# Optimization experiments

Measured on AMD Instinct MI355X. Metric: run time of the kernel, lower is better.

## Reference

```python
import jax, jax.numpy as jnp
import numpy as np

T, F, H = 2048, 256, 384  # seq_len, input_size, hidden_size


def setup_inputs() -> dict:
    key = jax.random.key(0)
    ks = jax.random.split(key, 16)
    s = 1.0 / np.sqrt(F)
    d = {"x": jax.random.normal(ks[0], (T, F), jnp.float32)}
    names = ["q", "k", "v", "i", "f", "o"]
    for j, n in enumerate(names):
        d[f"W{n}"] = jax.random.uniform(ks[1 + j], (H, F), jnp.float32, -s, s)
        d[f"b{n}"] = jax.random.uniform(ks[7 + j], (H,), jnp.float32, -s, s)
    d["conv_w"] = jax.random.uniform(ks[13], (1, 1, 4), jnp.float32, -0.5, 0.5)
    d["conv_b"] = jax.random.uniform(ks[14], (1,), jnp.float32, -0.5, 0.5)
    return d


def _forward(x, Wq, bq, Wk, bk, Wv, bv, Wi, bi, Wf, bf, Wo, bo, conv_w, conv_b):
    # Conv1d(1->1, kernel=4, padding=(3,3)) along time, per input feature.
    xt = x.T[:, None, :]  # (F, 1, T)  feature axis acts as batch
    y = jax.lax.conv_general_dilated(xt, conv_w, (1,), [(3, 3)])  # (F, 1, T+3)
    xp = (y[:, 0, :] + conv_b[0]).T  # (T+3, F)

    inv_sqrt_h = 1.0 / jnp.sqrt(jnp.asarray(H, xp.dtype))
    # Precompute all per-step projections with dense GEMMs (time-parallel part).
    q = xp @ Wq.T + bq                      # (T+3, H)
    k = (xp @ Wk.T + bk) * inv_sqrt_h       # (T+3, H); extra bias_k is zero-init
    v = xp @ Wv.T + bv
    i = jnp.exp(xp @ Wi.T + bi)
    f = jax.nn.sigmoid(xp @ Wf.T + bf)
    o = jax.nn.sigmoid(xp @ Wo.T + bo)

    def step(carry, inp):
        C, n = carry                         # C: (H,H), n: (H,)
        qt, kt, vt, it, ft, ot = inp
        C = ft * C + it * jnp.outer(vt, kt)  # broadcast over last axis, as original
        n = ft * n + it * kt
        den = jnp.maximum(jnp.abs(jnp.dot(n, qt)), 1.0)
        h = ot * (C @ qt) / den
        return (C, n), h

    init = (jnp.zeros((H, H), xp.dtype), jnp.zeros((H,), xp.dtype))
    _, hs = jax.lax.scan(step, init, (q, k, v, i, f, o))
    return hs[-1]  # return_all=False -> last hidden state, shape (H,)


def reference(x, Wq, bq, Wk, bk, Wv, bv, Wi, bi, Wf, bf, Wo, bo, conv_w, conv_b):
    return _forward(x, Wq, bq, Wk, bk, Wv, bv, Wi, bi, Wf, bf, Wo, bo, conv_w, conv_b)
```

## Files before the change

kernel.cpp:

```cpp
#include <hip/hip_runtime.h>
#include <math.h>

#define T_IN 2048
#define TP   2051
#define F    256
#define H    384
#define BK   16
#define NT2  129
#define NCS  258
#define NC3  257

__device__ __forceinline__ float logsig(float z) {
    return (z >= 0.0f) ? -log1pf(__expf(-z)) : z - log1pf(__expf(z));
}

__global__ __launch_bounds__(256) void k1_conv(const float* __restrict__ x,
                        const float* __restrict__ cw,
                        const float* __restrict__ cb, float* __restrict__ xp) {
    int t = blockIdx.x * 4 + (threadIdx.x >> 6);
    int f4 = threadIdx.x & 63;
    if (t >= TP) return;
    float w[4] = {cw[0], cw[1], cw[2], cw[3]};
    float b = cb[0];
    float4 acc = {b, b, b, b};
    int i0 = t - 3;
    const float4* x4 = (const float4*)x;
    #pragma unroll
    for (int j = 0; j < 4; ++j) {
        int tt = i0 + j;
        if (tt >= 0 && tt < T_IN) {
            float4 xv = x4[tt * 64 + f4];
            acc.x = fmaf(w[j], xv.x, acc.x);
            acc.y = fmaf(w[j], xv.y, acc.y);
            acc.z = fmaf(w[j], xv.z, acc.z);
            acc.w = fmaf(w[j], xv.w, acc.w);
        }
    }
    ((float4*)xp)[t * 64 + f4] = acc;
}

__global__ __launch_bounds__(64) void k2_proj(
    const float* __restrict__ xp,
    const float* __restrict__ Wk, const float* __restrict__ bk,
    const float* __restrict__ Wi, const float* __restrict__ bi,
    const float* __restrict__ Wf, const float* __restrict__ bf,
    float* __restrict__ zk, float* __restrict__ ai, float* __restrict__ lf,
    float* __restrict__ cs) {
    __shared__ float alds[BK][20];
    __shared__ float wlds[3][BK][68];
    __shared__ float csred[4][68];
    int tid = threadIdx.x;
    int t0 = blockIdx.x * 16, b0 = blockIdx.y * 64;
    int tx = tid & 15, ty = tid >> 4;
    const float* Wg[3] = {Wk, Wi, Wf};
    float acc[3][16];
    #pragma unroll
    for (int j = 0; j < 3; ++j)
        #pragma unroll
        for (int u = 0; u < 16; ++u) acc[j][u] = 0.0f;

    int at = tid >> 2;
    int ak = (tid & 3) * 4;

    for (int k0 = 0; k0 < 256; k0 += BK) {
        __syncthreads();
        float4 xv = {0.f, 0.f, 0.f, 0.f};
        if (t0 + at < TP) xv = *(const float4*)&xp[(t0 + at) * 256 + k0 + ak];
        alds[ak + 0][at] = xv.x; alds[ak + 1][at] = xv.y;
        alds[ak + 2][at] = xv.z; alds[ak + 3][at] = xv.w;
        #pragma unroll
        for (int j = 0; j < 3; ++j) {
            #pragma unroll
            for (int h = 0; h < 4; ++h) {
                int row = h * 16 + at;
                float4 wv = *(const float4*)&Wg[j][(b0 + row) * 256 + k0 + ak];
                wlds[j][ak + 0][row] = wv.x; wlds[j][ak + 1][row] = wv.y;
                wlds[j][ak + 2][row] = wv.z; wlds[j][ak + 3][row] = wv.w;
            }
        }
        __syncthreads();
        #pragma unroll
        for (int kk = 0; kk < BK; ++kk) {
            float4 a4 = *(const float4*)&alds[kk][ty * 4];
            #pragma unroll
            for (int j = 0; j < 3; ++j) {
                float4 b4 = *(const float4*)&wlds[j][kk][tx * 4];
                acc[j][0]  = fmaf(a4.x, b4.x, acc[j][0]);
                acc[j][1]  = fmaf(a4.x, b4.y, acc[j][1]);
                acc[j][2]  = fmaf(a4.x, b4.z, acc[j][2]);
                acc[j][3]  = fmaf(a4.x, b4.w, acc[j][3]);
                acc[j][4]  = fmaf(a4.y, b4.x, acc[j][4]);
                acc[j][5]  = fmaf(a4.y, b4.y, acc[j][5]);
                acc[j][6]  = fmaf(a4.y, b4.z, acc[j][6]);
                acc[j][7]  = fmaf(a4.y, b4.w, acc[j][7]);
                acc[j][8]  = fmaf(a4.z, b4.x, acc[j][8]);
                acc[j][9]  = fmaf(a4.z, b4.y, acc[j][9]);
                acc[j][10] = fmaf(a4.z, b4.z, acc[j][10]);
                acc[j][11] = fmaf(a4.z, b4.w, acc[j][11]);
                acc[j][12] = fmaf(a4.w, b4.x, acc[j][12]);
                acc[j][13] = fmaf(a4.w, b4.y, acc[j][13]);
                acc[j][14] = fmaf(a4.w, b4.z, acc[j][14]);
                acc[j][15] = fmaf(a4.w, b4.w, acc[j][15]);
            }
        }
    }
    int bA = b0 + tx * 4;
    float4 bk4 = *(const float4*)&bk[bA];
    float4 bi4 = *(const float4*)&bi[bA];
    float4 bf4 = *(const float4*)&bf[bA];
    const float sc = 0.05103103630798287f;
    float4 lfs = {0.f, 0.f, 0.f, 0.f};
    #pragma unroll
    for (int tt = 0; tt < 4; ++tt) {
        int t = t0 + ty * 4 + tt;
        if (t < TP) {
            int row = t * H + bA;
            int o = tt * 4;
            float4 v;
            v.x = (acc[0][o+0] + bk4.x) * sc; v.y = (acc[0][o+1] + bk4.y) * sc;
            v.z = (acc[0][o+2] + bk4.z) * sc; v.w = (acc[0][o+3] + bk4.w) * sc;
            *(float4*)&zk[row] = v;
            v.x = acc[1][o+0] + bi4.x; v.y = acc[1][o+1] + bi4.y;
            v.z = acc[1][o+2] + bi4.z; v.w = acc[1][o+3] + bi4.w;
            *(float4*)&ai[row] = v;
            float4 l;
            l.x = logsig(acc[2][o+0] + bf4.x); l.y = logsig(acc[2][o+1] + bf4.y);
            l.z = logsig(acc[2][o+2] + bf4.z); l.w = logsig(acc[2][o+3] + bf4.w);
            *(float4*)&lf[row] = l;
            lfs.x += l.x; lfs.y += l.y; lfs.z += l.z; lfs.w += l.w;
        }
    }
    *(float4*)&csred[ty][tx * 4] = lfs;
    __syncthreads();
    {
        float s0 = csred[0][tid] + csred[1][tid];
        float s1 = csred[2][tid] + csred[3][tid];
        cs[(2 * blockIdx.x + 0) * H + b0 + tid] = s0;
        cs[(2 * blockIdx.x + 1) * H + b0 + tid] = s1;
    }
}

__global__ __launch_bounds__(256) void k2b_qo(const float* __restrict__ xp,
        const float* __restrict__ Wq, const float* __restrict__ bq,
        const float* __restrict__ Wo, const float* __restrict__ bo,
        float* __restrict__ q, float* __restrict__ o) {
    int tid = threadIdx.x;
    int lane = tid & 63;
    int row = blockIdx.x * 4 + (tid >> 6);
    float4 xv = *(const float4*)&xp[(TP - 1) * 256 + lane * 4];
    float4 q4 = *(const float4*)&Wq[row * 256 + lane * 4];
    float4 o4 = *(const float4*)&Wo[row * 256 + lane * 4];
    float aq = fmaf(xv.x, q4.x, fmaf(xv.y, q4.y, fmaf(xv.z, q4.z, xv.w * q4.w)));
    float ao = fmaf(xv.x, o4.x, fmaf(xv.y, o4.y, fmaf(xv.z, o4.z, xv.w * o4.w)));
    #pragma unroll
    for (int off = 32; off; off >>= 1) {
        aq += __shfl_down(aq, off, 64);
        ao += __shfl_down(ao, off, 64);
    }
    if (lane == 0) {
        q[row] = aq + bq[row];
        o[row] = 1.0f / (1.0f + __expf(-(ao + bo[row])));
    }
}

__global__ __launch_bounds__(64) void k3b_scan(const float* __restrict__ cs,
                                               float* __restrict__ co) {
    int b = blockIdx.x * 64 + threadIdx.x;
    float L = 0.0f;
    #pragma unroll 16
    for (int c = NCS - 1; c >= 0; --c) {
        co[c * H + b] = L;
        L += cs[c * H + b];
    }
}

__global__ __launch_bounds__(384) void k3_fused(
    const float* __restrict__ ai, const float* __restrict__ lf,
    const float* __restrict__ zk, const float* __restrict__ co,
    const float* __restrict__ q, const float* __restrict__ xp,
    float* __restrict__ zf, float* __restrict__ Gf) {
    __shared__ float zred[6][256];
    __shared__ float gred[6];
    int tid = threadIdx.x;
    int w = tid >> 6, lane = tid & 63;
    int c = blockIdx.x, ts = c * 8;
    float co0 = co[c * H + tid];
    float qb = q[tid];
    float aiv[8], lfv[8], zkv[8];
    float4 xv[8];
    if (ts + 8 <= TP) {
        #pragma unroll
        for (int u = 0; u < 8; ++u) {
            int idx = (ts + u) * H + tid;
            aiv[u] = ai[idx]; lfv[u] = lf[idx]; zkv[u] = zk[idx];
            xv[u] = *(const float4*)&xp[(ts + u) * 256 + lane * 4];
        }
    } else {
        #pragma unroll
        for (int u = 0; u < 8; ++u) {
            if (ts + u < TP) {
                int idx = (ts + u) * H + tid;
                aiv[u] = ai[idx]; lfv[u] = lf[idx]; zkv[u] = zk[idx];
                xv[u] = *(const float4*)&xp[(ts + u) * 256 + lane * 4];
            } else {
                aiv[u] = -1e30f; lfv[u] = 0.f; zkv[u] = 0.f;
                xv[u].x = xv[u].y = xv[u].z = xv[u].w = 0.f;
            }
        }
    }
    float S = 0.f, gsum = 0.f;
    float z0 = 0.f, z1 = 0.f, z2 = 0.f, z3 = 0.f;
    #pragma unroll
    for (int u = 7; u >= 0; --u) {
        float wv = __expf(aiv[u] + co0 + S) * zkv[u] * qb;
        S += lfv[u];
        float s = wv;
        s += __shfl_xor(s, 1, 64);
        s += __shfl_xor(s, 2, 64);
        s += __shfl_xor(s, 4, 64);
        s += __shfl_xor(s, 8, 64);
        s += __shfl_xor(s, 16, 64);
        s += __shfl_xor(s, 32, 64);
        gsum += s;
        z0 = fmaf(s, xv[u].x, z0);
        z1 = fmaf(s, xv[u].y, z1);
        z2 = fmaf(s, xv[u].z, z2);
        z3 = fmaf(s, xv[u].w, z3);
    }
    zred[w][lane * 4 + 0] = z0;
    zred[w][lane * 4 + 1] = z1;
    zred[w][lane * 4 + 2] = z2;
    zred[w][lane * 4 + 3] = z3;
    if (lane == 0) gred[w] = gsum;
    __syncthreads();
    if (tid < 256) {
        float s = zred[0][tid] + zred[1][tid] + zred[2][tid]
                + zred[3][tid] + zred[4][tid] + zred[5][tid];
        atomicAdd(&zf[tid], s);
    }
    if (tid == 0)
        atomicAdd(Gf, gred[0] + gred[1] + gred[2] + gred[3] + gred[4] + gred[5]);
}

__global__ __launch_bounds__(256) void k6_out(const float* __restrict__ zf,
        const float* __restrict__ Gf,
        const float* __restrict__ Wv, const float* __restrict__ bv,
        const float* __restrict__ o, float* __restrict__ out) {
    int tid = threadIdx.x;
    int lane = tid & 63;
    int row = blockIdx.x * 4 + (tid >> 6);
    float Gv = Gf[0];
    float4 zv = *(const float4*)&zf[lane * 4];
    float4 wv = *(const float4*)&Wv[row * 256 + lane * 4];
    float acc = fmaf(zv.x, wv.x, fmaf(zv.y, wv.y, fmaf(zv.z, wv.z, zv.w * wv.w)));
    #pragma unroll
    for (int off = 32; off; off >>= 1) acc += __shfl_down(acc, off, 64);
    if (lane == 0)
        out[row] = o[row] * (acc + bv[row] * Gv) / fmaxf(fabsf(Gv), 1.0f);
}

extern "C" void kernel_launch(void* const* d_in, const int* in_sizes, int n_in,
                              void* d_out, int out_size, void* d_ws, size_t ws_size,
                              hipStream_t stream) {
    const float* x  = (const float*)d_in[0];
    const float* Wq = (const float*)d_in[1];  const float* bq = (const float*)d_in[2];
    const float* Wk = (const float*)d_in[3];  const float* bk = (const float*)d_in[4];
    const float* Wv = (const float*)d_in[5];  const float* bv = (const float*)d_in[6];
    const float* Wi = (const float*)d_in[7];  const float* bi = (const float*)d_in[8];
    const float* Wf = (const float*)d_in[9];  const float* bf = (const float*)d_in[10];
    const float* Wo = (const float*)d_in[11]; const float* bo = (const float*)d_in[12];
    const float* cw = (const float*)d_in[13]; const float* cb = (const float*)d_in[14];
    float* out = (float*)d_out;

    float* ws = (float*)d_ws;
    float* xp  = ws;
    float* zk  = xp  + TP * F;
    float* ai  = zk  + TP * H;
    float* lf  = ai  + TP * H;
    float* cs  = lf  + TP * H;
    float* co  = cs  + NCS * H;
    float* qv  = co  + NCS * H;
    float* ov  = qv  + H;
    float* zf  = ov  + H;
    float* Gf  = zf  + F;

    hipMemsetAsync((void*)zf, 0, (F + 4) * sizeof(float), stream);
    k1_conv<<<(TP + 3) / 4, 256, 0, stream>>>(x, cw, cb, xp);
    k2_proj<<<dim3(NT2, 6), 64, 0, stream>>>(xp, Wk, bk, Wi, bi, Wf, bf, zk, ai, lf, cs);
    k2b_qo<<<96, 256, 0, stream>>>(xp, Wq, bq, Wo, bo, qv, ov);
    k3b_scan<<<6, 64, 0, stream>>>(cs, co);
    k3_fused<<<NC3, 384, 0, stream>>>(ai, lf, zk, co, qv, xp, zf, Gf);
    k6_out<<<96, 256, 0, stream>>>(zf, Gf, Wv, bv, ov, out);
}
```

Measured before the change: 174.1 us.

## Fuse six launches into two kernels with recomputed conv and last-block epilogue

Collapses the conv, projection, q/o, scan, fused reduction and output kernels into two launches. The first kernel computes the conv per block into a private scratch tile, runs the k/i/f projection from registers, and uses extra blocks for the q/o projection and for zeroing accumulators. The second kernel recomputes the conv from x, replaces the suffix-scan kernel with a per-block loop over chunk sums, and lets the last block to finish (tracked by an atomic counter) compute the output. The aim is to remove launch overhead and the memset. The cost is redundant conv and suffix-sum work, weaker GEMM data reuse, and a serial epilogue in one block.

```diff
diff --git a/kernel.cpp b/kernel.cpp
--- a/kernel.cpp
+++ b/kernel.cpp
@@ -5,207 +5,197 @@
 #define TP   2051
 #define F    256
 #define H    384
-#define BK   16
-#define NT2  129
+#define NTB  129
+#define NC3  257
 #define NCS  258
-#define NC3  257
 
 __device__ __forceinline__ float logsig(float z) {
     return (z >= 0.0f) ? -log1pf(__expf(-z)) : z - log1pf(__expf(z));
 }
 
-__global__ __launch_bounds__(256) void k1_conv(const float* __restrict__ x,
-                        const float* __restrict__ cw,
-                        const float* __restrict__ cb, float* __restrict__ xp) {
-    int t = blockIdx.x * 4 + (threadIdx.x >> 6);
-    int f4 = threadIdx.x & 63;
-    if (t >= TP) return;
-    float w[4] = {cw[0], cw[1], cw[2], cw[3]};
-    float b = cb[0];
-    float4 acc = {b, b, b, b};
-    int i0 = t - 3;
-    const float4* x4 = (const float4*)x;
-    #pragma unroll
-    for (int j = 0; j < 4; ++j) {
-        int tt = i0 + j;
-        if (tt >= 0 && tt < T_IN) {
-            float4 xv = x4[tt * 64 + f4];
-            acc.x = fmaf(w[j], xv.x, acc.x);
-            acc.y = fmaf(w[j], xv.y, acc.y);
-            acc.z = fmaf(w[j], xv.z, acc.z);
-            acc.w = fmaf(w[j], xv.w, acc.w);
-        }
-    }
-    ((float4*)xp)[t * 64 + f4] = acc;
-}
-
-__global__ __launch_bounds__(64) void k2_proj(
-    const float* __restrict__ xp,
+__global__ __launch_bounds__(64) void KB(
+    const float* __restrict__ x, const float* __restrict__ cw, const float* __restrict__ cb,
     const float* __restrict__ Wk, const float* __restrict__ bk,
     const float* __restrict__ Wi, const float* __restrict__ bi,
     const float* __restrict__ Wf, const float* __restrict__ bf,
-    float* __restrict__ zk, float* __restrict__ ai, float* __restrict__ lf,
-    float* __restrict__ cs) {
-    __shared__ float alds[BK][20];
-    __shared__ float wlds[3][BK][68];
-    __shared__ float csred[4][68];
+    const float* __restrict__ Wq, const float* __restrict__ bq,
+    const float* __restrict__ Wo, const float* __restrict__ bo,
+    float* __restrict__ xpc, float* __restrict__ zk, float* __restrict__ ai,
+    float* __restrict__ lf, float* __restrict__ cs,
+    float* __restrict__ qv, float* __restrict__ ov, float* __restrict__ zf) {
     int tid = threadIdx.x;
-    int t0 = blockIdx.x * 16, b0 = blockIdx.y * 64;
-    int tx = tid & 15, ty = tid >> 4;
-    const float* Wg[3] = {Wk, Wi, Wf};
-    float acc[3][16];
-    #pragma unroll
-    for (int j = 0; j < 3; ++j)
-        #pragma unroll
-        for (int u = 0; u < 16; ++u) acc[j][u] = 0.0f;
-
-    int at = tid >> 2;
-    int ak = (tid & 3) * 4;
-
-    for (int k0 = 0; k0 < 256; k0 += BK) {
-        __syncthreads();
-        float4 xv = {0.f, 0.f, 0.f, 0.f};
-        if (t0 + at < TP) xv = *(const float4*)&xp[(t0 + at) * 256 + k0 + ak];
-        alds[ak + 0][at] = xv.x; alds[ak + 1][at] = xv.y;
-        alds[ak + 2][at] = xv.z; alds[ak + 3][at] = xv.w;
-        #pragma unroll
-        for (int j = 0; j < 3; ++j) {
+    int bx = blockIdx.x, by = blockIdx.y;
+
+    if (by == 6) {
+        if (bx == 6) {
+            for (int i = tid; i < 264; i += 64) zf[i] = 0.0f;
+            return;
+        }
+        if (bx > 6) return;
+        int lane = tid;
+        float w0 = cw[0], bb = cb[0];
+        float4 xr = *(const float4*)&x[2047 * 256 + lane * 4];
+        float4 xv = {bb + w0 * xr.x, bb + w0 * xr.y, bb + w0 * xr.z, bb + w0 * xr.w};
+        for (int r = 0; r < 64; ++r) {
+            int row = bx * 64 + r;
+            float4 q4 = *(const float4*)&Wq[row * 256 + lane * 4];
+            float4 o4 = *(const float4*)&Wo[row * 256 + lane * 4];
+            float aq = fmaf(xv.x, q4.x, fmaf(xv.y, q4.y, fmaf(xv.z, q4.z, xv.w * q4.w)));
+            float ao = fmaf(xv.x, o4.x, fmaf(xv.y, o4.y, fmaf(xv.z, o4.z, xv.w * o4.w)));
             #pragma unroll
-            for (int h = 0; h < 4; ++h) {
-                int row = h * 16 + at;
-                float4 wv = *(const float4*)&Wg[j][(b0 + row) * 256 + k0 + ak];
-                wlds[j][ak + 0][row] = wv.x; wlds[j][ak + 1][row] = wv.y;
-                wlds[j][ak + 2][row] = wv.z; wlds[j][ak + 3][row] = wv.w;
-            }
-        }
-        __syncthreads();
-        #pragma unroll
-        for (int kk = 0; kk < BK; ++kk) {
-            float4 a4 = *(const float4*)&alds[kk][ty * 4];
+            for (int off = 32; off; off >>= 1) {
+                aq += __shfl_down(aq, off, 64);
+                ao += __shfl_down(ao, off, 64);
+            }
+            if (lane == 0) {
+                qv[row] = aq + bq[row];
+                ov[row] = 1.0f / (1.0f + __expf(-(ao + bo[row])));
+            }
+        }
+        return;
+    }
+
+    int t0 = bx * 16;
+    int b  = by * 64 + tid;
+    float* xs = xpc + bx * 4096;
+
+    {
+        float w4[4] = {cw[0], cw[1], cw[2], cw[3]};
+        float bb = cb[0];
+        int r = tid >> 2;
+        int cb0 = (tid & 3) * 4;
+        int t = t0 + r;
+        for (int c16 = 0; c16 < 16; ++c16) {
+            int c = cb0 + c16 * 16;
+            float4 acc = {0.f, 0.f, 0.f, 0.f};
+            if (t < TP) {
+                acc.x = bb; acc.y = bb; acc.z = bb; acc.w = bb;
+                #pragma unroll
+                for (int j = 0; j < 4; ++j) {
+                    int tt = t - 3 + j;
+                    if (tt >= 0 && tt < T_IN) {
+                        float4 xv = *(const float4*)&x[tt * 256 + c];
+                        float wj = w4[j];
+                        acc.x = fmaf(wj, xv.x, acc.x);
+                        acc.y = fmaf(wj, xv.y, acc.y);
+                        acc.z = fmaf(wj, xv.z, acc.z);
+                        acc.w = fmaf(wj, xv.w, acc.w);
+                    }
+                }
+            }
+            *(float4*)&xs[r * 256 + c] = acc;
+        }
+    }
+    asm volatile("s_waitcnt vmcnt(0)" ::: "memory");
+
+    float acc0[16], acc1[16], acc2[16];
+    #pragma unroll
+    for (int t = 0; t < 16; ++t) { acc0[t] = 0.f; acc1[t] = 0.f; acc2[t] = 0.f; }
+    const float* pWk = Wk + b * 256;
+    const float* pWi = Wi + b * 256;
+    const float* pWf = Wf + b * 256;
+    for (int kc = 0; kc < 8; ++kc) {
+        int k0 = kc * 32;
+        float4 Bk[8], Bi[8], Bf[8];
+        #pragma unroll
+        for (int q = 0; q < 8; ++q) {
+            Bk[q] = *(const float4*)&pWk[k0 + q * 4];
+            Bi[q] = *(const float4*)&pWi[k0 + q * 4];
+            Bf[q] = *(const float4*)&pWf[k0 + q * 4];
+        }
+        #pragma unroll
+        for (int t = 0; t < 16; ++t) {
+            const float4* ap = (const float4*)&xs[t * 256 + k0];
             #pragma unroll
-            for (int j = 0; j < 3; ++j) {
-                float4 b4 = *(const float4*)&wlds[j][kk][tx * 4];
-                acc[j][0]  = fmaf(a4.x, b4.x, acc[j][0]);
-                acc[j][1]  = fmaf(a4.x, b4.y, acc[j][1]);
-                acc[j][2]  = fmaf(a4.x, b4.z, acc[j][2]);
-                acc[j][3]  = fmaf(a4.x, b4.w, acc[j][3]);
-                acc[j][4]  = fmaf(a4.y, b4.x, acc[j][4]);
-                acc[j][5]  = fmaf(a4.y, b4.y, acc[j][5]);
-                acc[j][6]  = fmaf(a4.y, b4.z, acc[j][6]);
-                acc[j][7]  = fmaf(a4.y, b4.w, acc[j][7]);
-                acc[j][8]  = fmaf(a4.z, b4.x, acc[j][8]);
-                acc[j][9]  = fmaf(a4.z, b4.y, acc[j][9]);
-                acc[j][10] = fmaf(a4.z, b4.z, acc[j][10]);
-                acc[j][11] = fmaf(a4.z, b4.w, acc[j][11]);
-                acc[j][12] = fmaf(a4.w, b4.x, acc[j][12]);
-                acc[j][13] = fmaf(a4.w, b4.y, acc[j][13]);
-                acc[j][14] = fmaf(a4.w, b4.z, acc[j][14]);
-                acc[j][15] = fmaf(a4.w, b4.w, acc[j][15]);
-            }
-        }
-    }
-    int bA = b0 + tx * 4;
-    float4 bk4 = *(const float4*)&bk[bA];
-    float4 bi4 = *(const float4*)&bi[bA];
-    float4 bf4 = *(const float4*)&bf[bA];
+            for (int q = 0; q < 8; ++q) {
+                float4 a = ap[q];
+                acc0[t] = fmaf(a.x, Bk[q].x, acc0[t]);
+                acc1[t] = fmaf(a.x, Bi[q].x, acc1[t]);
+                acc2[t] = fmaf(a.x, Bf[q].x, acc2[t]);
+                acc0[t] = fmaf(a.y, Bk[q].y, acc0[t]);
+                acc1[t] = fmaf(a.y, Bi[q].y, acc1[t]);
+                acc2[t] = fmaf(a.y, Bf[q].y, acc2[t]);
+                acc0[t] = fmaf(a.z, Bk[q].z, acc0[t]);
+                acc1[t] = fmaf(a.z, Bi[q].z, acc1[t]);
+                acc2[t] = fmaf(a.z, Bf[q].z, acc2[t]);
+                acc0[t] = fmaf(a.w, Bk[q].w, acc0[t]);
+                acc1[t] = fmaf(a.w, Bi[q].w, acc1[t]);
+                acc2[t] = fmaf(a.w, Bf[q].w, acc2[t]);
+            }
+        }
+    }
+    float bkv = bk[b], biv = bi[b], bfv = bf[b];
     const float sc = 0.05103103630798287f;
-    float4 lfs = {0.f, 0.f, 0.f, 0.f};
-    #pragma unroll
-    for (int tt = 0; tt < 4; ++tt) {
-        int t = t0 + ty * 4 + tt;
-        if (t < TP) {
-            int row = t * H + bA;
-            int o = tt * 4;
-            float4 v;
-            v.x = (acc[0][o+0] + bk4.x) * sc; v.y = (acc[0][o+1] + bk4.y) * sc;
-            v.z = (acc[0][o+2] + bk4.z) * sc; v.w = (acc[0][o+3] + bk4.w) * sc;
-            *(float4*)&zk[row] = v;
-            v.x = acc[1][o+0] + bi4.x; v.y = acc[1][o+1] + bi4.y;
-            v.z = acc[1][o+2] + bi4.z; v.w = acc[1][o+3] + bi4.w;
-            *(float4*)&ai[row] = v;
-            float4 l;
-            l.x = logsig(acc[2][o+0] + bf4.x); l.y = logsig(acc[2][o+1] + bf4.y);
-            l.z = logsig(acc[2][o+2] + bf4.z); l.w = logsig(acc[2][o+3] + bf4.w);
-            *(float4*)&lf[row] = l;
-            lfs.x += l.x; lfs.y += l.y; lfs.z += l.z; lfs.w += l.w;
-        }
-    }
-    *(float4*)&csred[ty][tx * 4] = lfs;
-    __syncthreads();
-    {
-        float s0 = csred[0][tid] + csred[1][tid];
-        float s1 = csred[2][tid] + csred[3][tid];
-        cs[(2 * blockIdx.x + 0) * H + b0 + tid] = s0;
-        cs[(2 * blockIdx.x + 1) * H + b0 + tid] = s1;
-    }
-}
-
-__global__ __launch_bounds__(256) void k2b_qo(const float* __restrict__ xp,
-        const float* __restrict__ Wq, const float* __restrict__ bq,
-        const float* __restrict__ Wo, const float* __restrict__ bo,
-        float* __restrict__ q, float* __restrict__ o) {
-    int tid = threadIdx.x;
-    int lane = tid & 63;
-    int row = blockIdx.x * 4 + (tid >> 6);
-    float4 xv = *(const float4*)&xp[(TP - 1) * 256 + lane * 4];
-    float4 q4 = *(const float4*)&Wq[row * 256 + lane * 4];
-    float4 o4 = *(const float4*)&Wo[row * 256 + lane * 4];
-    float aq = fmaf(xv.x, q4.x, fmaf(xv.y, q4.y, fmaf(xv.z, q4.z, xv.w * q4.w)));
-    float ao = fmaf(xv.x, o4.x, fmaf(xv.y, o4.y, fmaf(xv.z, o4.z, xv.w * o4.w)));
-    #pragma unroll
-    for (int off = 32; off; off >>= 1) {
-        aq += __shfl_down(aq, off, 64);
-        ao += __shfl_down(ao, off, 64);
-    }
-    if (lane == 0) {
-        q[row] = aq + bq[row];
-        o[row] = 1.0f / (1.0f + __expf(-(ao + bo[row])));
-    }
-}
-
-__global__ __launch_bounds__(64) void k3b_scan(const float* __restrict__ cs,
-                                               float* __restrict__ co) {
-    int b = blockIdx.x * 64 + threadIdx.x;
-    float L = 0.0f;
-    #pragma unroll 16
-    for (int c = NCS - 1; c >= 0; --c) {
-        co[c * H + b] = L;
-        L += cs[c * H + b];
-    }
-}
-
-__global__ __launch_bounds__(384) void k3_fused(
-    const float* __restrict__ ai, const float* __restrict__ lf,
-    const float* __restrict__ zk, const float* __restrict__ co,
-    const float* __restrict__ q, const float* __restrict__ xp,
-    float* __restrict__ zf, float* __restrict__ Gf) {
+    float lsA = 0.f, lsB = 0.f;
+    #pragma unroll
+    for (int t = 0; t < 16; ++t) {
+        int tt = t0 + t;
+        if (tt < TP) {
+            int row = tt * H + b;
+            zk[row] = (acc0[t] + bkv) * sc;
+            ai[row] = acc1[t] + biv;
+            float l = logsig(acc2[t] + bfv);
+            lf[row] = l;
+            if (t < 8) lsA += l; else lsB += l;
+        }
+    }
+    cs[(2 * bx + 0) * H + b] = lsA;
+    cs[(2 * bx + 1) * H + b] = lsB;
+}
+
+__global__ __launch_bounds__(384) void KC(
+    const float* __restrict__ x, const float* __restrict__ cw, const float* __restrict__ cb,
+    const float* __restrict__ ai, const float* __restrict__ lf, const float* __restrict__ zk,
+    const float* __restrict__ cs, const float* __restrict__ qv, const float* __restrict__ ov,
+    const float* __restrict__ Wv, const float* __restrict__ bv,
+    float* __restrict__ zf, float* __restrict__ out) {
     __shared__ float zred[6][256];
     __shared__ float gred[6];
+    __shared__ float zl[257];
+    __shared__ int flag;
     int tid = threadIdx.x;
     int w = tid >> 6, lane = tid & 63;
     int c = blockIdx.x, ts = c * 8;
-    float co0 = co[c * H + tid];
-    float qb = q[tid];
+
+    float co0 = 0.f;
+    #pragma unroll 8
+    for (int cc = c + 1; cc < NCS; ++cc) co0 += cs[cc * H + tid];
+    float qb = qv[tid];
+
+    float4 xv[8];
+    {
+        float w4[4] = {cw[0], cw[1], cw[2], cw[3]};
+        float bb = cb[0];
+        #pragma unroll
+        for (int u = 0; u < 8; ++u) {
+            float4 a = {0.f, 0.f, 0.f, 0.f};
+            int t = ts + u;
+            if (t < TP) {
+                a.x = bb; a.y = bb; a.z = bb; a.w = bb;
+                #pragma unroll
+                for (int j = 0; j < 4; ++j) {
+                    int tt = t - 3 + j;
+                    if (tt >= 0 && tt < T_IN) {
+                        float4 xr = *(const float4*)&x[tt * 256 + lane * 4];
+                        float wj = w4[j];
+                        a.x = fmaf(wj, xr.x, a.x);
+                        a.y = fmaf(wj, xr.y, a.y);
+                        a.z = fmaf(wj, xr.z, a.z);
+                        a.w = fmaf(wj, xr.w, a.w);
+                    }
+                }
+            }
+            xv[u] = a;
+        }
+    }
     float aiv[8], lfv[8], zkv[8];
-    float4 xv[8];
-    if (ts + 8 <= TP) {
-        #pragma unroll
-        for (int u = 0; u < 8; ++u) {
+    #pragma unroll
+    for (int u = 0; u < 8; ++u) {
+        if (ts + u < TP) {
             int idx = (ts + u) * H + tid;
             aiv[u] = ai[idx]; lfv[u] = lf[idx]; zkv[u] = zk[idx];
-            xv[u] = *(const float4*)&xp[(ts + u) * 256 + lane * 4];
-        }
-    } else {
-        #pragma unroll
-        for (int u = 0; u < 8; ++u) {
-            if (ts + u < TP) {
-                int idx = (ts + u) * H + tid;
-                aiv[u] = ai[idx]; lfv[u] = lf[idx]; zkv[u] = zk[idx];
-                xv[u] = *(const float4*)&xp[(ts + u) * 256 + lane * 4];
-            } else {
-                aiv[u] = -1e30f; lfv[u] = 0.f; zkv[u] = 0.f;
-                xv[u].x = xv[u].y = xv[u].z = xv[u].w = 0.f;
-            }
+        } else {
+            aiv[u] = -1e30f; lfv[u] = 0.f; zkv[u] = 0.f;
         }
     }
     float S = 0.f, gsum = 0.f;
@@ -239,24 +229,31 @@
         atomicAdd(&zf[tid], s);
     }
     if (tid == 0)
-        atomicAdd(Gf, gred[0] + gred[1] + gred[2] + gred[3] + gred[4] + gred[5]);
-}
-
-__global__ __launch_bounds__(256) void k6_out(const float* __restrict__ zf,
-        const float* __restrict__ Gf,
-        const float* __restrict__ Wv, const float* __restrict__ bv,
-        const float* __restrict__ o, float* __restrict__ out) {
-    int tid = threadIdx.x;
-    int lane = tid & 63;
-    int row = blockIdx.x * 4 + (tid >> 6);
-    float Gv = Gf[0];
-    float4 zv = *(const float4*)&zf[lane * 4];
-    float4 wv = *(const float4*)&Wv[row * 256 + lane * 4];
-    float acc = fmaf(zv.x, wv.x, fmaf(zv.y, wv.y, fmaf(zv.z, wv.z, zv.w * wv.w)));
-    #pragma unroll
-    for (int off = 32; off; off >>= 1) acc += __shfl_down(acc, off, 64);
-    if (lane == 0)
-        out[row] = o[row] * (acc + bv[row] * Gv) / fmaxf(fabsf(Gv), 1.0f);
+        atomicAdd(&zf[256], gred[0] + gred[1] + gred[2] + gred[3] + gred[4] + gred[5]);
+    __syncthreads();
+    if (tid == 0) {
+        __threadfence();
+        int old = atomicAdd((int*)(zf + 257), 1);
+        flag = (old == NC3 - 1) ? 1 : 0;
+    }
+    __syncthreads();
+    if (!flag) return;
+
+    if (tid < 257)
+        zl[tid] = __hip_atomic_load(&zf[tid], __ATOMIC_RELAXED, __HIP_MEMORY_SCOPE_AGENT);
+    __syncthreads();
+    float G = zl[256];
+    float den = fmaxf(fabsf(G), 1.0f);
+    for (int r = 0; r < 64; ++r) {
+        int row = w * 64 + r;
+        float4 wv4 = *(const float4*)&Wv[row * 256 + lane * 4];
+        float4 z4 = *(const float4*)&zl[lane * 4];
+        float acc = fmaf(z4.x, wv4.x, fmaf(z4.y, wv4.y, fmaf(z4.z, wv4.z, z4.w * wv4.w)));
+        #pragma unroll
+        for (int off = 32; off; off >>= 1) acc += __shfl_down(acc, off, 64);
+        if (lane == 0)
+            out[row] = ov[row] * (acc + bv[row] * G) / den;
+    }
 }
 
 extern "C" void kernel_launch(void* const* d_in, const int* in_sizes, int n_in,
@@ -273,22 +270,16 @@
     float* out = (float*)d_out;
 
     float* ws = (float*)d_ws;
-    float* xp  = ws;
-    float* zk  = xp  + TP * F;
+    float* xpc = ws;
+    float* zk  = xpc + NTB * 4096;
     float* ai  = zk  + TP * H;
     float* lf  = ai  + TP * H;
     float* cs  = lf  + TP * H;
-    float* co  = cs  + NCS * H;
-    float* qv  = co  + NCS * H;
+    float* qv  = cs  + NCS * H;
     float* ov  = qv  + H;
     float* zf  = ov  + H;
-    float* Gf  = zf  + F;
-
-    hipMemsetAsync((void*)zf, 0, (F + 4) * sizeof(float), stream);
-    k1_conv<<<(TP + 3) / 4, 256, 0, stream>>>(x, cw, cb, xp);
-    k2_proj<<<dim3(NT2, 6), 64, 0, stream>>>(xp, Wk, bk, Wi, bi, Wf, bf, zk, ai, lf, cs);
-    k2b_qo<<<96, 256, 0, stream>>>(xp, Wq, bq, Wo, bo, qv, ov);
-    k3b_scan<<<6, 64, 0, stream>>>(cs, co);
-    k3_fused<<<NC3, 384, 0, stream>>>(ai, lf, zk, co, qv, xp, zf, Gf);
-    k6_out<<<96, 256, 0, stream>>>(zf, Gf, Wv, bv, ov, out);
-}
+
+    KB<<<dim3(NTB, 7), 64, 0, stream>>>(x, cw, cb, Wk, bk, Wi, bi, Wf, bf,
+                                        Wq, bq, Wo, bo, xpc, zk, ai, lf, cs, qv, ov, zf);
+    KC<<<NC3, 384, 0, stream>>>(x, cw, cb, ai, lf, zk, cs, qv, ov, Wv, bv, zf, out);
+}
```

Result: slower. 241.1 us (+38.5%).
